# Performance work log

Hardware: AMD Instinct MI355X
Metric: run time of the kernel (lower is better)

## Reference

```python
import jax, jax.numpy as jnp
import numpy as np

H = 1024   # hidden_size
V = 32000  # output_size (vocab)
S = 4096   # encoder seq_len
L = 1      # n_layers


def setup_inputs() -> dict:
    key = jax.random.key(0)
    ks = jax.random.split(key, 12)
    scale = 0.02
    return {
        "word_input": jax.random.randint(ks[0], (1,), 0, V),
        "last_hidden": jax.random.normal(ks[1], (L, 1, H), jnp.float32),
        "encoder_hiddens": jax.random.normal(ks[2], (S, 1, H), jnp.float32),
        "embedding": jax.random.normal(ks[3], (V, H), jnp.float32) * scale,
        "w_ih": jax.random.normal(ks[4], (3 * H, H), jnp.float32) * scale,
        "w_hh": jax.random.normal(ks[5], (3 * H, H), jnp.float32) * scale,
        "b_ih": jax.random.normal(ks[6], (3 * H,), jnp.float32) * scale,
        "b_hh": jax.random.normal(ks[7], (3 * H,), jnp.float32) * scale,
        "attn_w": jax.random.normal(ks[8], (H, H), jnp.float32) * scale,
        "attn_b": jax.random.normal(ks[9], (H,), jnp.float32) * scale,
        "out_w": jax.random.normal(ks[10], (V, 2 * H), jnp.float32) * scale,
        "out_b": jax.random.normal(ks[11], (V,), jnp.float32) * scale,
    }


def reference(word_input, last_hidden, encoder_hiddens, embedding,
              w_ih, w_hh, b_ih, b_hh, attn_w, attn_b, out_w, out_b):
    h_dim = embedding.shape[1]
    # embedding lookup -> GRU single step (PyTorch GRU cell math)
    x = embedding[word_input[0]]            # [H]
    h0 = last_hidden[0, 0]                  # [H]
    gx = w_ih @ x + b_ih                    # [3H]
    gh = w_hh @ h0 + b_hh                   # [3H]
    r = jax.nn.sigmoid(gx[:h_dim] + gh[:h_dim])
    z = jax.nn.sigmoid(gx[h_dim:2 * h_dim] + gh[h_dim:2 * h_dim])
    n = jnp.tanh(gx[2 * h_dim:] + r * gh[2 * h_dim:])
    h = (1.0 - z) * n + z * h0              # rnn_output / new hidden [H]
    # Bahdanau-style scores: dot(hidden, attn(enc_i)) for all i, batched
    enc = encoder_hiddens[:, 0, :]          # [S, H]
    scores = (enc @ attn_w.T + attn_b) @ h  # [S]
    attn = jax.nn.softmax(scores)           # [S]
    context = attn @ enc                    # [H]
    output = jnp.concatenate([h, context]) @ out_w.T + out_b  # [V]
    return (output[None, :], h[None, None, :], attn[None, None, :])
```

## Files before the change

### kernel.cpp

```cpp
#include <hip/hip_runtime.h>
#include <cstddef>

#define Hn 1024
#define Vn 32000
#define Sn 4096
#define CSHIFT 20.0f

__device__ __forceinline__ float wave_reduce_sum(float v) {
#pragma unroll
    for (int o = 32; o > 0; o >>= 1) v += __shfl_down(v, o, 64);
    return v;
}


__device__ __forceinline__ void out_h_rows(const float* __restrict__ out_w,
                                           const float* __restrict__ out_b,
                                           const float* __restrict__ ws_h,
                                           float* __restrict__ out,
                                           int row_base, int t)
{
    __shared__ float c[Hn];
    ((float4*)c)[t] = ((const float4*)ws_h)[t];
    __syncthreads();
    const int wv = t >> 6, lane = t & 63;
    const int row = row_base + wv;
    const float* w = out_w + (size_t)row * (2 * Hn);
    float acc = 0.f;
#pragma unroll
    for (int k = 0; k < 4; ++k) {
        const int idx = k * 256 + lane * 4;
        const float4 w4 = *(const float4*)(w + idx);
        acc += w4.x * c[idx] + w4.y * c[idx + 1] + w4.z * c[idx + 2] + w4.w * c[idx + 3];
    }
    acc = wave_reduce_sum(acc);
    if (lane == 0) out[row] = acc + out_b[row];
}

__global__ __launch_bounds__(256) void k_gru(const int* __restrict__ word,
                                             const float* __restrict__ emb,
                                             const float* __restrict__ h0,
                                             const float* __restrict__ w_ih,
                                             const float* __restrict__ w_hh,
                                             const float* __restrict__ b_ih,
                                             const float* __restrict__ b_hh,
                                             float* __restrict__ ws_h,
                                             float* __restrict__ ws_denom,
                                             float* __restrict__ out_h)
{
    const int k = blockIdx.x;
    const int t = threadIdx.x;

    if (k == 0 && t == 0) ws_denom[0] = 0.f;

    const float* x = emb + (size_t)word[0] * Hn;
    const float4 xv = ((const float4*)x)[t];
    const float4 hv = ((const float4*)h0)[t];

    float acc[6];
    const float* rows[6] = {
        w_ih + (size_t)k * Hn, w_ih + (size_t)(k + Hn) * Hn, w_ih + (size_t)(k + 2 * Hn) * Hn,
        w_hh + (size_t)k * Hn, w_hh + (size_t)(k + Hn) * Hn, w_hh + (size_t)(k + 2 * Hn) * Hn
    };
#pragma unroll
    for (int g = 0; g < 6; ++g) {
        const float4 w = ((const float4*)rows[g])[t];
        const float4 vv = (g < 3) ? xv : hv;
        acc[g] = w.x * vv.x + w.y * vv.y + w.z * vv.z + w.w * vv.w;
    }

    __shared__ float red[6][4];
    const int wv = t >> 6, lane = t & 63;
#pragma unroll
    for (int g = 0; g < 6; ++g) {
        const float s = wave_reduce_sum(acc[g]);
        if (lane == 0) red[g][wv] = s;
    }
    __syncthreads();
    if (t == 0) {
        float g0 = red[0][0] + red[0][1] + red[0][2] + red[0][3] + b_ih[k];
        float g1 = red[1][0] + red[1][1] + red[1][2] + red[1][3] + b_ih[k + Hn];
        float g2 = red[2][0] + red[2][1] + red[2][2] + red[2][3] + b_ih[k + 2 * Hn];
        float g3 = red[3][0] + red[3][1] + red[3][2] + red[3][3] + b_hh[k];
        float g4 = red[4][0] + red[4][1] + red[4][2] + red[4][3] + b_hh[k + Hn];
        float g5 = red[5][0] + red[5][1] + red[5][2] + red[5][3] + b_hh[k + 2 * Hn];
        float r = 1.f / (1.f + expf(-(g0 + g3)));
        float z = 1.f / (1.f + expf(-(g1 + g4)));
        float n = tanhf(g2 + r * g5);
        float hk = (1.f - z) * n + z * h0[k];
        ws_h[k]  = hk;
        out_h[k] = hk;
    }
}

__global__ __launch_bounds__(256) void k_a(const float* __restrict__ attn_w,
                                           const float* __restrict__ ws_h,
                                           float* __restrict__ v,
                                           const float* __restrict__ out_w,
                                           const float* __restrict__ out_b,
                                           float* __restrict__ out)
{
    const int t = threadIdx.x, bid = blockIdx.x;
    if (bid < 64) {
        const int tj = t >> 4, tk = t & 15;
        const int k = bid * 16 + tk;
        float acc = 0.f;
        for (int j = tj; j < Hn; j += 16)
            acc += attn_w[(size_t)j * Hn + k] * ws_h[j];
        __shared__ float p[16][17];
        p[tj][tk] = acc;
        __syncthreads();
        if (t < 16) {
            float s = 0.f;
#pragma unroll
            for (int j = 0; j < 16; ++j) s += p[j][t];
            v[bid * 16 + t] = s;
        }
    } else {
        out_h_rows(out_w, out_b, ws_h, out, (bid - 64) * 4, t);
    }
}

__global__ __launch_bounds__(256) void k_sctx(const float* __restrict__ enc,
                                              const float* __restrict__ ws_v,
                                              float* __restrict__ escore,
                                              float* __restrict__ part,
                                              float* __restrict__ denom,
                                              const float* __restrict__ ws_h,
                                              const float* __restrict__ out_w,
                                              const float* __restrict__ out_b,
                                              float* __restrict__ out)
{
    const int t = threadIdx.x, bid = blockIdx.x;
    if (bid < 256) {
        __shared__ float rows[16][Hn];
        __shared__ float vsh[Hn];
        __shared__ float es[16];
        const int wv = t >> 6, lane = t & 63;
        const int s0 = bid * 16;

        ((float4*)vsh)[t] = ((const float4*)ws_v)[t];
        const float* erow = enc + (size_t)s0 * Hn;
#pragma unroll
        for (int r = 0; r < 16; ++r)
            ((float4*)rows[r])[t] = ((const float4*)(erow + (size_t)r * Hn))[t];
        __syncthreads();

#pragma unroll
        for (int q = 0; q < 4; ++q) {
            const int r = wv * 4 + q;
            float a = 0.f;
#pragma unroll
            for (int k = 0; k < 4; ++k) {
                const int idx = k * 256 + lane * 4;
                const float4 e = *(const float4*)&rows[r][idx];
                a += e.x * vsh[idx] + e.y * vsh[idx + 1] + e.z * vsh[idx + 2] + e.w * vsh[idx + 3];
            }
            a = wave_reduce_sum(a);
            if (lane == 0) {
                const float ev = expf(a - CSHIFT);
                es[r] = ev;
                escore[s0 + r] = ev;
            }
        }
        __syncthreads();
        if (t == 0) {
            float d = 0.f;
#pragma unroll
            for (int r = 0; r < 16; ++r) d += es[r];
            atomicAdd(denom, d);
        }
        float4 acc = make_float4(0.f, 0.f, 0.f, 0.f);
#pragma unroll
        for (int r = 0; r < 16; ++r) {
            const float a = es[r];
            const float4 e = ((const float4*)rows[r])[t];
            acc.x += a * e.x; acc.y += a * e.y; acc.z += a * e.z; acc.w += a * e.w;
        }
        ((float4*)(part + (size_t)bid * Hn))[t] = acc;
    } else {
        out_h_rows(out_w, out_b, ws_h, out, 10668 + (bid - 256) * 4, t);
    }
}

__global__ __launch_bounds__(256) void k_red(const float* __restrict__ part,
                                             float* __restrict__ ctx,
                                             const float* __restrict__ escore,
                                             const float* __restrict__ denom,
                                             float* __restrict__ out_attn,
                                             const float* __restrict__ ws_h,
                                             const float* __restrict__ out_w,
                                             const float* __restrict__ out_b,
                                             float* __restrict__ out)
{
    const int t = threadIdx.x, bid = blockIdx.x;
    if (bid < 4) {
        const int j = bid * 256 + t;
        float acc = 0.f;
        for (int pb = 0; pb < 256; ++pb)
            acc += part[(size_t)pb * Hn + j];
        ctx[j] = acc;
    } else if (bid < 8) {
        const float inv = 1.f / denom[0];
        const int s = (bid - 4) * 1024 + t * 4;
        const float4 e = *(const float4*)(escore + s);
        *(float4*)(out_attn + s) = make_float4(e.x * inv, e.y * inv, e.z * inv, e.w * inv);
    } else {
        out_h_rows(out_w, out_b, ws_h, out, 21336 + (bid - 8) * 4, t);
    }
}

__global__ __launch_bounds__(256) void k_tail(const float* __restrict__ out_w,
                                              const float* __restrict__ ws_ctx,
                                              const float* __restrict__ denom,
                                              float* __restrict__ out)
{
    __shared__ float c[Hn];
    const int t = threadIdx.x;
    ((float4*)c)[t] = ((const float4*)ws_ctx)[t];
    __syncthreads();
    const int wv = t >> 6, lane = t & 63;
    const int row = blockIdx.x * 4 + wv;
    const float* w = out_w + (size_t)row * (2 * Hn) + Hn;
    float acc = 0.f;
#pragma unroll
    for (int k = 0; k < 4; ++k) {
        const int idx = k * 256 + lane * 4;
        const float4 w4 = *(const float4*)(w + idx);
        acc += w4.x * c[idx] + w4.y * c[idx + 1] + w4.z * c[idx + 2] + w4.w * c[idx + 3];
    }
    acc = wave_reduce_sum(acc);
    if (lane == 0) out[row] += acc * (1.f / denom[0]);
}

extern "C" void kernel_launch(void* const* d_in, const int* in_sizes, int n_in,
                              void* d_out, int out_size, void* d_ws, size_t ws_size,
                              hipStream_t stream) {
    const int*   word   = (const int*)d_in[0];
    const float* h_last = (const float*)d_in[1];
    const float* enc    = (const float*)d_in[2];
    const float* emb    = (const float*)d_in[3];
    const float* w_ih   = (const float*)d_in[4];
    const float* w_hh   = (const float*)d_in[5];
    const float* b_ih   = (const float*)d_in[6];
    const float* b_hh   = (const float*)d_in[7];
    const float* attn_w = (const float*)d_in[8];
    const float* out_w  = (const float*)d_in[10];
    const float* out_b  = (const float*)d_in[11];
    float* out = (float*)d_out;
    float* ws  = (float*)d_ws;

    float* ws_h      = ws;
    float* ws_ctx    = ws + 1024;
    float* ws_v      = ws + 2048;
    float* ws_escore = ws + 3072;
    float* ws_denom  = ws + 7168;
    float* ws_part   = ws + 8192;
    float* out_h     = out + Vn;
    float* out_attn  = out + Vn + Hn;

    k_gru<<<Hn, 256, 0, stream>>>(word, emb, h_last, w_ih, w_hh, b_ih, b_hh, ws_h, ws_denom, out_h);
    k_a<<<64 + 2667, 256, 0, stream>>>(attn_w, ws_h, ws_v, out_w, out_b, out);
    k_sctx<<<256 + 2667, 256, 0, stream>>>(enc, ws_v, ws_escore, ws_part, ws_denom,
                                           ws_h, out_w, out_b, out);
    k_red<<<8 + 2666, 256, 0, stream>>>(ws_part, ws_ctx, ws_escore, ws_denom, out_attn,
                                        ws_h, out_w, out_b, out);
    k_tail<<<Vn / 4, 256, 0, stream>>>(out_w, ws_ctx, ws_denom, out);
}
```

Measured before the change: 94.70 us.

## Accumulate attention context via atomics instead of partial buffer reduction

The score/context kernel now handles 32 encoder rows per block in a loop of 4-row groups, using a much smaller shared buffer. Each block atomically adds its weighted context into a zeroed ctx buffer, so the 256x1024 partials array and the serial reduction blocks in k_red go away. The cost is 128x1024 float atomics, nondeterministic summation order, and an extra zeroing pass in k_gru. The block count also drops, so each block does more sequential work with more syncthreads.

```diff
diff --git a/kernel.cpp b/kernel.cpp
--- a/kernel.cpp
+++ b/kernel.cpp
@@ -44,13 +44,18 @@
                                              const float* __restrict__ b_ih,
                                              const float* __restrict__ b_hh,
                                              float* __restrict__ ws_h,
+                                             float* __restrict__ ws_ctx,
                                              float* __restrict__ ws_denom,
                                              float* __restrict__ out_h)
 {
     const int k = blockIdx.x;
     const int t = threadIdx.x;
 
-    if (k == 0 && t == 0) ws_denom[0] = 0.f;
+    if (k == 0) {
+#pragma unroll
+        for (int i = 0; i < 4; ++i) ws_ctx[t + i * 256] = 0.f;
+        if (t == 0) ws_denom[0] = 0.f;
+    }
 
     const float* x = emb + (size_t)word[0] * Hn;
     const float4 xv = ((const float4*)x)[t];
@@ -123,7 +128,7 @@
 __global__ __launch_bounds__(256) void k_sctx(const float* __restrict__ enc,
                                               const float* __restrict__ ws_v,
                                               float* __restrict__ escore,
-                                              float* __restrict__ part,
+                                              float* __restrict__ ctx,
                                               float* __restrict__ denom,
                                               const float* __restrict__ ws_h,
                                               const float* __restrict__ out_w,
@@ -131,60 +136,63 @@
                                               float* __restrict__ out)
 {
     const int t = threadIdx.x, bid = blockIdx.x;
-    if (bid < 256) {
-        __shared__ float rows[16][Hn];
+    if (bid < 128) {
+        __shared__ float rows[4][Hn];
         __shared__ float vsh[Hn];
-        __shared__ float es[16];
+        __shared__ float esl[4];
         const int wv = t >> 6, lane = t & 63;
-        const int s0 = bid * 16;
+        const int s0 = bid * 32;
 
         ((float4*)vsh)[t] = ((const float4*)ws_v)[t];
-        const float* erow = enc + (size_t)s0 * Hn;
-#pragma unroll
-        for (int r = 0; r < 16; ++r)
-            ((float4*)rows[r])[t] = ((const float4*)(erow + (size_t)r * Hn))[t];
-        __syncthreads();
-
-#pragma unroll
-        for (int q = 0; q < 4; ++q) {
-            const int r = wv * 4 + q;
+
+        float4 acc = make_float4(0.f, 0.f, 0.f, 0.f);
+        float dsum = 0.f;
+
+        for (int g = 0; g < 8; ++g) {
+            __syncthreads();
+            const float* erow = enc + (size_t)(s0 + g * 4) * Hn;
+#pragma unroll
+            for (int r = 0; r < 4; ++r)
+                ((float4*)rows[r])[t] = ((const float4*)(erow + (size_t)r * Hn))[t];
+            __syncthreads();
+
             float a = 0.f;
 #pragma unroll
             for (int k = 0; k < 4; ++k) {
                 const int idx = k * 256 + lane * 4;
-                const float4 e = *(const float4*)&rows[r][idx];
+                const float4 e = *(const float4*)&rows[wv][idx];
                 a += e.x * vsh[idx] + e.y * vsh[idx + 1] + e.z * vsh[idx + 2] + e.w * vsh[idx + 3];
             }
             a = wave_reduce_sum(a);
             if (lane == 0) {
                 const float ev = expf(a - CSHIFT);
-                es[r] = ev;
-                escore[s0 + r] = ev;
+                esl[wv] = ev;
+                escore[s0 + g * 4 + wv] = ev;
             }
+            __syncthreads();
+
+            const float e0 = esl[0], e1 = esl[1], e2 = esl[2], e3 = esl[3];
+            dsum += e0 + e1 + e2 + e3;
+            const float4 r0 = ((const float4*)rows[0])[t];
+            const float4 r1 = ((const float4*)rows[1])[t];
+            const float4 r2 = ((const float4*)rows[2])[t];
+            const float4 r3 = ((const float4*)rows[3])[t];
+            acc.x += e0 * r0.x + e1 * r1.x + e2 * r2.x + e3 * r3.x;
+            acc.y += e0 * r0.y + e1 * r1.y + e2 * r2.y + e3 * r3.y;
+            acc.z += e0 * r0.z + e1 * r1.z + e2 * r2.z + e3 * r3.z;
+            acc.w += e0 * r0.w + e1 * r1.w + e2 * r2.w + e3 * r3.w;
         }
-        __syncthreads();
-        if (t == 0) {
-            float d = 0.f;
-#pragma unroll
-            for (int r = 0; r < 16; ++r) d += es[r];
-            atomicAdd(denom, d);
-        }
-        float4 acc = make_float4(0.f, 0.f, 0.f, 0.f);
-#pragma unroll
-        for (int r = 0; r < 16; ++r) {
-            const float a = es[r];
-            const float4 e = ((const float4*)rows[r])[t];
-            acc.x += a * e.x; acc.y += a * e.y; acc.z += a * e.z; acc.w += a * e.w;
-        }
-        ((float4*)(part + (size_t)bid * Hn))[t] = acc;
+        atomicAdd(&ctx[t * 4],     acc.x);
+        atomicAdd(&ctx[t * 4 + 1], acc.y);
+        atomicAdd(&ctx[t * 4 + 2], acc.z);
+        atomicAdd(&ctx[t * 4 + 3], acc.w);
+        if (t == 0) atomicAdd(denom, dsum);
     } else {
-        out_h_rows(out_w, out_b, ws_h, out, 10668 + (bid - 256) * 4, t);
-    }
-}
-
-__global__ __launch_bounds__(256) void k_red(const float* __restrict__ part,
-                                             float* __restrict__ ctx,
-                                             const float* __restrict__ escore,
+        out_h_rows(out_w, out_b, ws_h, out, 10668 + (bid - 128) * 4, t);
+    }
+}
+
+__global__ __launch_bounds__(256) void k_red(const float* __restrict__ escore,
                                              const float* __restrict__ denom,
                                              float* __restrict__ out_attn,
                                              const float* __restrict__ ws_h,
@@ -194,18 +202,12 @@
 {
     const int t = threadIdx.x, bid = blockIdx.x;
     if (bid < 4) {
-        const int j = bid * 256 + t;
-        float acc = 0.f;
-        for (int pb = 0; pb < 256; ++pb)
-            acc += part[(size_t)pb * Hn + j];
-        ctx[j] = acc;
-    } else if (bid < 8) {
         const float inv = 1.f / denom[0];
-        const int s = (bid - 4) * 1024 + t * 4;
+        const int s = bid * 1024 + t * 4;
         const float4 e = *(const float4*)(escore + s);
         *(float4*)(out_attn + s) = make_float4(e.x * inv, e.y * inv, e.z * inv, e.w * inv);
     } else {
-        out_h_rows(out_w, out_b, ws_h, out, 21336 + (bid - 8) * 4, t);
+        out_h_rows(out_w, out_b, ws_h, out, 21336 + (bid - 4) * 4, t);
     }
 }
 
@@ -216,6 +218,7 @@
 {
     __shared__ float c[Hn];
     const int t = threadIdx.x;
+    const float inv = 1.f / denom[0];
     ((float4*)c)[t] = ((const float4*)ws_ctx)[t];
     __syncthreads();
     const int wv = t >> 6, lane = t & 63;
@@ -229,7 +232,7 @@
         acc += w4.x * c[idx] + w4.y * c[idx + 1] + w4.z * c[idx + 2] + w4.w * c[idx + 3];
     }
     acc = wave_reduce_sum(acc);
-    if (lane == 0) out[row] += acc * (1.f / denom[0]);
+    if (lane == 0) out[row] += acc * inv;
 }
 
 extern "C" void kernel_launch(void* const* d_in, const int* in_sizes, int n_in,
@@ -254,15 +257,15 @@
     float* ws_v      = ws + 2048;
     float* ws_escore = ws + 3072;
     float* ws_denom  = ws + 7168;
-    float* ws_part   = ws + 8192;
     float* out_h     = out + Vn;
     float* out_attn  = out + Vn + Hn;
 
-    k_gru<<<Hn, 256, 0, stream>>>(word, emb, h_last, w_ih, w_hh, b_ih, b_hh, ws_h, ws_denom, out_h);
+    k_gru<<<Hn, 256, 0, stream>>>(word, emb, h_last, w_ih, w_hh, b_ih, b_hh,
+                                  ws_h, ws_ctx, ws_denom, out_h);
     k_a<<<64 + 2667, 256, 0, stream>>>(attn_w, ws_h, ws_v, out_w, out_b, out);
-    k_sctx<<<256 + 2667, 256, 0, stream>>>(enc, ws_v, ws_escore, ws_part, ws_denom,
+    k_sctx<<<128 + 2667, 256, 0, stream>>>(enc, ws_v, ws_escore, ws_ctx, ws_denom,
                                            ws_h, out_w, out_b, out);
-    k_red<<<8 + 2666, 256, 0, stream>>>(ws_part, ws_ctx, ws_escore, ws_denom, out_attn,
+    k_red<<<4 + 2666, 256, 0, stream>>>(ws_escore, ws_denom, out_attn,
                                         ws_h, out_w, out_b, out);
     k_tail<<<Vn / 4, 256, 0, stream>>>(out_w, ws_ctx, ws_denom, out);
 }
```

Measured after the change: 95.21 us. No clear change (+0.5%).
